# Performance work log

Measured on AMD Instinct MI355X. Metric: run time of the kernel, lower is better.

## Reference

```python
import jax, jax.numpy as jnp
import numpy as np

N_NODES = 50000
N_EDGES = 800000
IN_DIM = 128
ATT_DIM = 128
NEG_SLOPE = 0.01  # nn.LeakyReLU default


def setup_inputs() -> dict:
    key = jax.random.key(0)
    ks = jax.random.split(key, 8)
    x = jax.random.normal(ks[0], (N_NODES, IN_DIM), dtype=jnp.float32)
    src_idx = jax.random.randint(ks[1], (N_EDGES,), 0, N_NODES, dtype=jnp.int32)
    dst_idx = jax.random.randint(ks[2], (N_EDGES,), 0, N_NODES, dtype=jnp.int32)
    # small init scale keeps exp(score) numerically tame
    src_w = jax.random.normal(ks[3], (IN_DIM, ATT_DIM), dtype=jnp.float32) * 0.05
    src_b = jnp.zeros((ATT_DIM,), dtype=jnp.float32)
    dst_w = jax.random.normal(ks[4], (IN_DIM, ATT_DIM), dtype=jnp.float32) * 0.05
    dst_b = jnp.zeros((ATT_DIM,), dtype=jnp.float32)
    att_w = jax.random.normal(ks[5], (ATT_DIM, 1), dtype=jnp.float32) * 0.05
    att_b = jnp.zeros((1,), dtype=jnp.float32)
    return {"x": x, "src_idx": src_idx, "dst_idx": dst_idx,
            "src_w": src_w, "src_b": src_b, "dst_w": dst_w, "dst_b": dst_b,
            "att_w": att_w, "att_b": att_b}


def reference(x, src_idx, dst_idx, src_w, src_b, dst_w, dst_b, att_w, att_b):
    n = x.shape[0]
    # 1) mean aggregation of source features onto destinations (copy_u + mean)
    deg = jax.ops.segment_sum(jnp.ones_like(dst_idx, dtype=x.dtype), dst_idx, num_segments=n)
    h_mean = jax.ops.segment_sum(x[src_idx], dst_idx, num_segments=n)
    h_mean = h_mean / jnp.maximum(deg, 1.0)[:, None]
    # 2) attention projections on nodes (dense GEMMs)
    ha_src = x @ src_w + src_b          # [N, att_dim]
    ha_dst = h_mean @ dst_w + dst_b     # [N, att_dim]
    # 3) per-edge u_add_v -> LeakyReLU -> att Linear -> exp
    e = jax.nn.leaky_relu(ha_src[src_idx] + ha_dst[dst_idx], NEG_SLOPE)  # [E, att_dim]
    s = jnp.exp(e @ att_w + att_b)      # [E, 1]
    # 4) edge softmax: normalize by segment sum over destination
    denom = jax.ops.segment_sum(s, dst_idx, num_segments=n)  # [N, 1]
    a = s / denom[dst_idx]              # [E, 1]
    # 5) u_mul_e weighted aggregation (sum)
    out = jax.ops.segment_sum(x[src_idx] * a, dst_idx, num_segments=n)  # [N, in_dim]
    return out
```

## Files before the change

kernel.cpp:

```cpp
#include <hip/hip_runtime.h>
#include <math.h>

#define N_NODES 50000
#define N_EDGES 800000
#define DIM 128
#define NEG_SLOPE 0.01f
#define CAP 64
#define DEGS 32

#define GEMM_BLOCKS 3125
#define SCAT_BLOCKS 3125

typedef short v8s __attribute__((ext_vector_type(8)));
typedef float v4f __attribute__((ext_vector_type(4)));

__device__ inline unsigned f2bf2(float a, float b) {
    unsigned ua = __float_as_uint(a);
    unsigned ub = __float_as_uint(b);
    ua = (ua + 0x7fffu + ((ua >> 16) & 1u)) >> 16;
    ub = (ub + 0x7fffu + ((ub >> 16) & 1u)) & 0xffff0000u;
    return ua | ub;
}
__device__ inline float2 bf2f(unsigned u) {
    float2 r;
    r.x = __uint_as_float(u << 16);
    r.y = __uint_as_float(u & 0xffff0000u);
    return r;
}

__device__ inline float2 pka(float2 a, float2 b) {
    return make_float2(a.x + b.x, a.y + b.y);
}
__device__ inline float2 pkfma(float2 a, float2 b, float2 c) {
    return make_float2(fmaf(a.x, b.x, c.x), fmaf(a.y, b.y, c.y));
}
__device__ inline float2 leaky2(float2 v) {
    return make_float2(fmaxf(v.x, v.x * NEG_SLOPE), fmaxf(v.y, v.y * NEG_SLOPE));
}

#define ROR_ADD(v, CTRL) \
    ((v) + __int_as_float(__builtin_amdgcn_update_dpp( \
        0, __float_as_int(v), (CTRL), 0xf, 0xf, false)))

__global__ __launch_bounds__(256) void k_prepw(
    const float* __restrict__ src_w, const float* __restrict__ dst_w,
    unsigned* __restrict__ whT, int* __restrict__ deg)
{
    int gid = blockIdx.x * 256 + threadIdx.x;
    if (gid < 256 * 64) {
        int n = gid >> 6;
        int kk = gid & 63;
        const float* W = (n < 128) ? src_w : dst_w;
        int col = n & 127;
        float w0 = W[(2 * kk) * DIM + col];
        float w1 = W[(2 * kk + 1) * DIM + col];
        whT[gid] = f2bf2(w0, w1);
    }
    if (gid < N_NODES) deg[gid * DEGS] = 0;
}

__global__ __launch_bounds__(256) void k_scatter(
    const int* __restrict__ src, const int* __restrict__ dst,
    int* __restrict__ deg, int* __restrict__ slots)
{
    int e = blockIdx.x * 256 + threadIdx.x;
    int s = src[e];
    int d = dst[e];
    int pos = atomicAdd(&deg[d * DEGS], 1);
    if (pos < CAP) slots[d * CAP + pos] = s * 64;
}

__global__ __launch_bounds__(64) void k_gemm(
    const float* __restrict__ x, const unsigned* __restrict__ whT,
    const float* __restrict__ src_b, unsigned* __restrict__ hx_u,
    unsigned* __restrict__ yu)
{
    __shared__ unsigned L[16][132];
    int bx = blockIdx.x;
    int lane = threadIdx.x;
    int quad = lane >> 4;
    int m = lane & 15;

    int arow = bx * 16 + m;
    const float4* xp = (const float4*)(x + (size_t)arow * DIM + quad * 8);
    float4 f[4][2];
    #pragma unroll
    for (int k0 = 0; k0 < 4; ++k0) {
        f[k0][0] = xp[k0 * 8];
        f[k0][1] = xp[k0 * 8 + 1];
    }

    v8s b[4];
    #pragma unroll
    for (int k0 = 0; k0 < 4; ++k0) {
        union { unsigned u[4]; v8s s; } pk;
        pk.u[0] = f2bf2(f[k0][0].x, f[k0][0].y);
        pk.u[1] = f2bf2(f[k0][0].z, f[k0][0].w);
        pk.u[2] = f2bf2(f[k0][1].x, f[k0][1].y);
        pk.u[3] = f2bf2(f[k0][1].z, f[k0][1].w);
        b[k0] = pk.s;
        int c = k0 * 32 + quad * 8 + 1;
        L[m][c + 0] = pk.u[0];
        L[m][c + 2] = pk.u[1];
        L[m][c + 4] = pk.u[2];
        L[m][c + 6] = pk.u[3];
    }

    v4f yacc[8];
    #pragma unroll
    for (int nt = 0; nt < 16; ++nt) {
        v4f acc = {0.f, 0.f, 0.f, 0.f};
        const uint4* ap = (const uint4*)(whT + (size_t)(nt * 16 + m) * 64 + quad * 4);
        #pragma unroll
        for (int k0 = 0; k0 < 4; ++k0) {
            union { uint4 u; v8s s; } af;
            af.u = ap[k0 * 4];
            acc = __builtin_amdgcn_mfma_f32_16x16x32_bf16(af.s, b[k0], acc, 0, 0, 0);
        }
        if (nt < 8) {
            float4 bia = ((const float4*)src_b)[nt * 4 + quad];
            int c = nt * 16 + quad * 4;
            L[m][c]     = f2bf2(acc[0] + bia.x, acc[1] + bia.y);
            L[m][c + 2] = f2bf2(acc[2] + bia.z, acc[3] + bia.w);
        } else {
            yacc[nt - 8] = acc;
        }
    }

    int rbase0 = bx * 16;
    for (int i = lane; i < 512; i += 64) {
        int r = i >> 5, c = i & 31;
        ((uint4*)(hx_u + (size_t)(rbase0 + r) * 128))[c] = *(const uint4*)&L[r][c * 4];
    }

    #pragma unroll
    for (int t = 0; t < 8; ++t) {
        int c = t * 8 + quad * 2;
        L[m][c]     = f2bf2(yacc[t][0], yacc[t][1]);
        L[m][c + 1] = f2bf2(yacc[t][2], yacc[t][3]);
    }
    for (int i = lane; i < 256; i += 64) {
        int r = i >> 4, c = i & 15;
        ((uint4*)(yu + (size_t)(rbase0 + r) * 64))[c] = *(const uint4*)&L[r][c * 4];
    }
}

__global__ __launch_bounds__(256) void k_fuse(
    const uint2* __restrict__ hx, const unsigned* __restrict__ yu,
    const int* __restrict__ slots, const int* __restrict__ deg,
    const float* __restrict__ dst_b, const float* __restrict__ att_w,
    const float* __restrict__ att_b, float* __restrict__ out)
{
    int g = blockIdx.x * 256 + threadIdx.x;
    int node = g >> 6;
    int lane = g & 63;
    int grp = lane >> 4;
    int sl = lane & 15;
    int cnt = deg[node * DEGS];
    if (cnt == 0) {
        if (grp < 2) {
            v4f z = {0.f, 0.f, 0.f, 0.f};
            __builtin_nontemporal_store(z, (v4f*)out + node * 32 + (grp ? 16 + sl : sl));
        }
        return;
    }
    int cc = (cnt < CAP) ? cnt : CAP;
    int trips = (cc + 3) >> 2;
    int myoff = (lane < cc) ? slots[node * CAP + lane] : 0;

    float2 hd01 = {0.f, 0.f}, hd23 = {0.f, 0.f};
    float2 hd45 = {0.f, 0.f}, hd67 = {0.f, 0.f};
    #pragma unroll 4
    for (int t = 0; t < trips; ++t) {
        int i = 4 * t + grp;
        bool valid = (i < cc);
        int off = __shfl(myoff, valid ? i : 0);
        if (valid) {
            const uint2* yp = (const uint2*)(yu + off);
            uint2 qa = yp[sl];
            uint2 qb = yp[16 + sl];
            hd01 = pka(hd01, bf2f(qa.x));
            hd23 = pka(hd23, bf2f(qa.y));
            hd45 = pka(hd45, bf2f(qb.x));
            hd67 = pka(hd67, bf2f(qb.y));
        }
    }
    float inv = 1.0f / (float)cnt;
    #define XRED(f) { f += __shfl_xor(f, 32); f += __shfl_xor(f, 16); f *= inv; }
    XRED(hd01.x) XRED(hd01.y) XRED(hd23.x) XRED(hd23.y)
    XRED(hd45.x) XRED(hd45.y) XRED(hd67.x) XRED(hd67.y)
    #undef XRED
    float4 db0 = ((const float4*)dst_b)[sl];
    float4 db1 = ((const float4*)dst_b)[16 + sl];
    hd01.x += db0.x; hd01.y += db0.y; hd23.x += db0.z; hd23.y += db0.w;
    hd45.x += db1.x; hd45.y += db1.y; hd67.x += db1.z; hd67.y += db1.w;

    float4 aw0f = ((const float4*)att_w)[sl];
    float4 aw1f = ((const float4*)att_w)[16 + sl];
    float2 aw01 = make_float2(aw0f.x, aw0f.y), aw23 = make_float2(aw0f.z, aw0f.w);
    float2 aw45 = make_float2(aw1f.x, aw1f.y), aw67 = make_float2(aw1f.z, aw1f.w);
    float ab = att_b[0];
    float2 o01 = {0.f, 0.f}, o23 = {0.f, 0.f};
    float2 o45 = {0.f, 0.f}, o67 = {0.f, 0.f};
    float dsum = 0.f;
    #pragma unroll 4
    for (int t = 0; t < trips; ++t) {
        int i = 4 * t + grp;
        bool valid = (i < cc);
        int off = __shfl(myoff, valid ? i : 0);
        if (valid) {
            const uint4* hp = (const uint4*)(hx + off);
            uint4 qa = hp[sl];
            uint4 qb = hp[16 + sl];
            float2 p2 = {0.f, 0.f};
            p2 = pkfma(leaky2(pka(bf2f(qa.x), hd01)), aw01, p2);
            p2 = pkfma(leaky2(pka(bf2f(qa.z), hd23)), aw23, p2);
            p2 = pkfma(leaky2(pka(bf2f(qb.x), hd45)), aw45, p2);
            p2 = pkfma(leaky2(pka(bf2f(qb.z), hd67)), aw67, p2);
            float p = p2.x + p2.y;
            p = ROR_ADD(p, 0x128);
            p = ROR_ADD(p, 0x124);
            p = ROR_ADD(p, 0x122);
            p = ROR_ADD(p, 0x121);
            float s = __expf(p + ab);
            float2 s2 = make_float2(s, s);
            o01 = pkfma(bf2f(qa.y), s2, o01);
            o23 = pkfma(bf2f(qa.w), s2, o23);
            o45 = pkfma(bf2f(qb.y), s2, o45);
            o67 = pkfma(bf2f(qb.w), s2, o67);
            dsum += s;
        }
    }
    dsum += __shfl_xor(dsum, 32);
    dsum += __shfl_xor(dsum, 16);
    #define XRED2(f) { f += __shfl_xor(f, 32); f += __shfl_xor(f, 16); }
    XRED2(o01.x) XRED2(o01.y) XRED2(o23.x) XRED2(o23.y)
    XRED2(o45.x) XRED2(o45.y) XRED2(o67.x) XRED2(o67.y)
    #undef XRED2
    float r = 1.0f / dsum;
    if (grp < 2) {
        v4f ov;
        if (grp == 0) {
            ov[0] = o01.x * r; ov[1] = o01.y * r; ov[2] = o23.x * r; ov[3] = o23.y * r;
            __builtin_nontemporal_store(ov, (v4f*)out + node * 32 + sl);
        } else {
            ov[0] = o45.x * r; ov[1] = o45.y * r; ov[2] = o67.x * r; ov[3] = o67.y * r;
            __builtin_nontemporal_store(ov, (v4f*)out + node * 32 + 16 + sl);
        }
    }
}

extern "C" void kernel_launch(void* const* d_in, const int* in_sizes, int n_in,
                              void* d_out, int out_size, void* d_ws, size_t ws_size,
                              hipStream_t stream)
{
    const float* x     = (const float*)d_in[0];
    const int*   src   = (const int*)d_in[1];
    const int*   dst   = (const int*)d_in[2];
    const float* src_w = (const float*)d_in[3];
    const float* src_b = (const float*)d_in[4];
    const float* dst_w = (const float*)d_in[5];
    const float* dst_b = (const float*)d_in[6];
    const float* att_w = (const float*)d_in[7];
    const float* att_b = (const float*)d_in[8];
    float* out = (float*)d_out;
    (void)in_sizes; (void)n_in; (void)out_size; (void)ws_size;

    const size_t NF = (size_t)N_NODES * DIM;

    int* ws = (int*)d_ws;
    int* ideg  = ws;
    int* slots = ws + 1600512;
    unsigned* whT = (unsigned*)(ws + 4800512);
    unsigned* yu  = whT + 16384;
    uint2*    hx  = (uint2*)(yu + NF / 2);

    k_prepw<<<256, 256, 0, stream>>>(src_w, dst_w, whT, ideg);

    k_scatter<<<SCAT_BLOCKS, 256, 0, stream>>>(src, dst, ideg, slots);

    k_gemm<<<GEMM_BLOCKS, 64, 0, stream>>>(x, whT, src_b, (unsigned*)hx, yu);

    k_fuse<<<N_NODES * 64 / 256, 256, 0, stream>>>(
        hx, yu, slots, ideg, dst_b, att_w, att_b, out);
}
```

Baseline: 248.2 us.

## Merge weight prep into scatter kernel, memset degrees, use native packed vector math

Weight bf16 transposition now runs in the first 64 blocks of the scatter kernel, removing the separate prep kernel launch. The degree counters are zeroed with hipMemsetAsync instead, which clears the full strided array (about 6.4 MB) rather than only one int per node. The fused kernel's float2 helpers become ext_vector_type float2 with elementwise builtins, aimed at getting packed FP32 instructions (v_pk_fma/v_pk_add). The memset writes far more bytes than the old kernel did, which could offset the saved launch.

```diff
diff --git a/kernel.cpp b/kernel.cpp
--- a/kernel.cpp
+++ b/kernel.cpp
@@ -13,6 +13,7 @@
 
 typedef short v8s __attribute__((ext_vector_type(8)));
 typedef float v4f __attribute__((ext_vector_type(4)));
+typedef float v2f __attribute__((ext_vector_type(2)));
 
 __device__ inline unsigned f2bf2(float a, float b) {
     unsigned ua = __float_as_uint(a);
@@ -21,33 +22,30 @@
     ub = (ub + 0x7fffu + ((ub >> 16) & 1u)) & 0xffff0000u;
     return ua | ub;
 }
-__device__ inline float2 bf2f(unsigned u) {
-    float2 r;
+__device__ inline v2f bf2v(unsigned u) {
+    v2f r;
     r.x = __uint_as_float(u << 16);
     r.y = __uint_as_float(u & 0xffff0000u);
     return r;
 }
-
-__device__ inline float2 pka(float2 a, float2 b) {
-    return make_float2(a.x + b.x, a.y + b.y);
-}
-__device__ inline float2 pkfma(float2 a, float2 b, float2 c) {
-    return make_float2(fmaf(a.x, b.x, c.x), fmaf(a.y, b.y, c.y));
-}
-__device__ inline float2 leaky2(float2 v) {
-    return make_float2(fmaxf(v.x, v.x * NEG_SLOPE), fmaxf(v.y, v.y * NEG_SLOPE));
+__device__ inline v2f lk2(v2f v) {
+    return __builtin_elementwise_max(v, v * NEG_SLOPE);
 }
 
 #define ROR_ADD(v, CTRL) \
     ((v) + __int_as_float(__builtin_amdgcn_update_dpp( \
         0, __float_as_int(v), (CTRL), 0xf, 0xf, false)))
 
-__global__ __launch_bounds__(256) void k_prepw(
+__global__ __launch_bounds__(256) void k_scatter(
+    const int* __restrict__ src, const int* __restrict__ dst,
+    int* __restrict__ deg, int* __restrict__ slots,
     const float* __restrict__ src_w, const float* __restrict__ dst_w,
-    unsigned* __restrict__ whT, int* __restrict__ deg)
-{
-    int gid = blockIdx.x * 256 + threadIdx.x;
-    if (gid < 256 * 64) {
+    unsigned* __restrict__ whT)
+{
+    int bx = blockIdx.x;
+    int tid = threadIdx.x;
+    if (bx < 64) {
+        int gid = bx * 256 + tid;
         int n = gid >> 6;
         int kk = gid & 63;
         const float* W = (n < 128) ? src_w : dst_w;
@@ -56,14 +54,7 @@
         float w1 = W[(2 * kk + 1) * DIM + col];
         whT[gid] = f2bf2(w0, w1);
     }
-    if (gid < N_NODES) deg[gid * DEGS] = 0;
-}
-
-__global__ __launch_bounds__(256) void k_scatter(
-    const int* __restrict__ src, const int* __restrict__ dst,
-    int* __restrict__ deg, int* __restrict__ slots)
-{
-    int e = blockIdx.x * 256 + threadIdx.x;
+    int e = bx * 256 + tid;
     int s = src[e];
     int d = dst[e];
     int pos = atomicAdd(&deg[d * DEGS], 1);
@@ -168,8 +159,8 @@
     int trips = (cc + 3) >> 2;
     int myoff = (lane < cc) ? slots[node * CAP + lane] : 0;
 
-    float2 hd01 = {0.f, 0.f}, hd23 = {0.f, 0.f};
-    float2 hd45 = {0.f, 0.f}, hd67 = {0.f, 0.f};
+    v2f hd01 = {0.f, 0.f}, hd23 = {0.f, 0.f};
+    v2f hd45 = {0.f, 0.f}, hd67 = {0.f, 0.f};
     #pragma unroll 4
     for (int t = 0; t < trips; ++t) {
         int i = 4 * t + grp;
@@ -179,29 +170,32 @@
             const uint2* yp = (const uint2*)(yu + off);
             uint2 qa = yp[sl];
             uint2 qb = yp[16 + sl];
-            hd01 = pka(hd01, bf2f(qa.x));
-            hd23 = pka(hd23, bf2f(qa.y));
-            hd45 = pka(hd45, bf2f(qb.x));
-            hd67 = pka(hd67, bf2f(qb.y));
+            hd01 += bf2v(qa.x);
+            hd23 += bf2v(qa.y);
+            hd45 += bf2v(qb.x);
+            hd67 += bf2v(qb.y);
         }
     }
     float inv = 1.0f / (float)cnt;
+    float m0 = hd01.x, m1 = hd01.y, m2 = hd23.x, m3 = hd23.y;
+    float m4 = hd45.x, m5 = hd45.y, m6 = hd67.x, m7 = hd67.y;
     #define XRED(f) { f += __shfl_xor(f, 32); f += __shfl_xor(f, 16); f *= inv; }
-    XRED(hd01.x) XRED(hd01.y) XRED(hd23.x) XRED(hd23.y)
-    XRED(hd45.x) XRED(hd45.y) XRED(hd67.x) XRED(hd67.y)
+    XRED(m0) XRED(m1) XRED(m2) XRED(m3) XRED(m4) XRED(m5) XRED(m6) XRED(m7)
     #undef XRED
     float4 db0 = ((const float4*)dst_b)[sl];
     float4 db1 = ((const float4*)dst_b)[16 + sl];
-    hd01.x += db0.x; hd01.y += db0.y; hd23.x += db0.z; hd23.y += db0.w;
-    hd45.x += db1.x; hd45.y += db1.y; hd67.x += db1.z; hd67.y += db1.w;
+    hd01 = (v2f){m0 + db0.x, m1 + db0.y};
+    hd23 = (v2f){m2 + db0.z, m3 + db0.w};
+    hd45 = (v2f){m4 + db1.x, m5 + db1.y};
+    hd67 = (v2f){m6 + db1.z, m7 + db1.w};
 
     float4 aw0f = ((const float4*)att_w)[sl];
     float4 aw1f = ((const float4*)att_w)[16 + sl];
-    float2 aw01 = make_float2(aw0f.x, aw0f.y), aw23 = make_float2(aw0f.z, aw0f.w);
-    float2 aw45 = make_float2(aw1f.x, aw1f.y), aw67 = make_float2(aw1f.z, aw1f.w);
+    v2f aw01 = (v2f){aw0f.x, aw0f.y}, aw23 = (v2f){aw0f.z, aw0f.w};
+    v2f aw45 = (v2f){aw1f.x, aw1f.y}, aw67 = (v2f){aw1f.z, aw1f.w};
     float ab = att_b[0];
-    float2 o01 = {0.f, 0.f}, o23 = {0.f, 0.f};
-    float2 o45 = {0.f, 0.f}, o67 = {0.f, 0.f};
+    v2f o01 = {0.f, 0.f}, o23 = {0.f, 0.f};
+    v2f o45 = {0.f, 0.f}, o67 = {0.f, 0.f};
     float dsum = 0.f;
     #pragma unroll 4
     for (int t = 0; t < trips; ++t) {
@@ -212,39 +206,40 @@
             const uint4* hp = (const uint4*)(hx + off);
             uint4 qa = hp[sl];
             uint4 qb = hp[16 + sl];
-            float2 p2 = {0.f, 0.f};
-            p2 = pkfma(leaky2(pka(bf2f(qa.x), hd01)), aw01, p2);
-            p2 = pkfma(leaky2(pka(bf2f(qa.z), hd23)), aw23, p2);
-            p2 = pkfma(leaky2(pka(bf2f(qb.x), hd45)), aw45, p2);
-            p2 = pkfma(leaky2(pka(bf2f(qb.z), hd67)), aw67, p2);
+            v2f p2 = {0.f, 0.f};
+            p2 = __builtin_elementwise_fma(lk2(bf2v(qa.x) + hd01), aw01, p2);
+            p2 = __builtin_elementwise_fma(lk2(bf2v(qa.z) + hd23), aw23, p2);
+            p2 = __builtin_elementwise_fma(lk2(bf2v(qb.x) + hd45), aw45, p2);
+            p2 = __builtin_elementwise_fma(lk2(bf2v(qb.z) + hd67), aw67, p2);
             float p = p2.x + p2.y;
             p = ROR_ADD(p, 0x128);
             p = ROR_ADD(p, 0x124);
             p = ROR_ADD(p, 0x122);
             p = ROR_ADD(p, 0x121);
             float s = __expf(p + ab);
-            float2 s2 = make_float2(s, s);
-            o01 = pkfma(bf2f(qa.y), s2, o01);
-            o23 = pkfma(bf2f(qa.w), s2, o23);
-            o45 = pkfma(bf2f(qb.y), s2, o45);
-            o67 = pkfma(bf2f(qb.w), s2, o67);
+            v2f s2 = (v2f){s, s};
+            o01 = __builtin_elementwise_fma(bf2v(qa.y), s2, o01);
+            o23 = __builtin_elementwise_fma(bf2v(qa.w), s2, o23);
+            o45 = __builtin_elementwise_fma(bf2v(qb.y), s2, o45);
+            o67 = __builtin_elementwise_fma(bf2v(qb.w), s2, o67);
             dsum += s;
         }
     }
     dsum += __shfl_xor(dsum, 32);
     dsum += __shfl_xor(dsum, 16);
+    float r0 = o01.x, r1 = o01.y, r2 = o23.x, r3 = o23.y;
+    float r4 = o45.x, r5 = o45.y, r6 = o67.x, r7 = o67.y;
     #define XRED2(f) { f += __shfl_xor(f, 32); f += __shfl_xor(f, 16); }
-    XRED2(o01.x) XRED2(o01.y) XRED2(o23.x) XRED2(o23.y)
-    XRED2(o45.x) XRED2(o45.y) XRED2(o67.x) XRED2(o67.y)
+    XRED2(r0) XRED2(r1) XRED2(r2) XRED2(r3) XRED2(r4) XRED2(r5) XRED2(r6) XRED2(r7)
     #undef XRED2
     float r = 1.0f / dsum;
     if (grp < 2) {
         v4f ov;
         if (grp == 0) {
-            ov[0] = o01.x * r; ov[1] = o01.y * r; ov[2] = o23.x * r; ov[3] = o23.y * r;
+            ov[0] = r0 * r; ov[1] = r1 * r; ov[2] = r2 * r; ov[3] = r3 * r;
             __builtin_nontemporal_store(ov, (v4f*)out + node * 32 + sl);
         } else {
-            ov[0] = o45.x * r; ov[1] = o45.y * r; ov[2] = o67.x * r; ov[3] = o67.y * r;
+            ov[0] = r4 * r; ov[1] = r5 * r; ov[2] = r6 * r; ov[3] = r7 * r;
             __builtin_nontemporal_store(ov, (v4f*)out + node * 32 + 16 + sl);
         }
     }
@@ -275,9 +270,10 @@
     unsigned* yu  = whT + 16384;
     uint2*    hx  = (uint2*)(yu + NF / 2);
 
-    k_prepw<<<256, 256, 0, stream>>>(src_w, dst_w, whT, ideg);
-
-    k_scatter<<<SCAT_BLOCKS, 256, 0, stream>>>(src, dst, ideg, slots);
+    hipMemsetAsync(ideg, 0, (size_t)N_NODES * DEGS * sizeof(int), stream);
+
+    k_scatter<<<SCAT_BLOCKS, 256, 0, stream>>>(
+        src, dst, ideg, slots, src_w, dst_w, whT);
 
     k_gemm<<<GEMM_BLOCKS, 64, 0, stream>>>(x, whT, src_b, (unsigned*)hx, yu);
 
```

Result: no change. 246.8 us (-0.5%).
